# Performance work log

Measured on AMD Instinct MI355X. Metric: run time of the kernel, lower is better.

## Reference

```python
import jax, jax.numpy as jnp
import numpy as np

B, S, D_MODEL, H = 2, 2048, 1024, 16
HD = D_MODEL // H  # head_dim = 64


def setup_inputs() -> dict:
    key = jax.random.key(0)
    kx, kq, kk, kv, ko = jax.random.split(key, 5)
    scale = 1.0 / np.sqrt(D_MODEL)
    return {
        "x": jax.random.normal(kx, (B, S, D_MODEL), dtype=jnp.float32),
        "Wq": jax.random.normal(kq, (D_MODEL, D_MODEL), dtype=jnp.float32) * scale,
        "Wk": jax.random.normal(kk, (D_MODEL, D_MODEL), dtype=jnp.float32) * scale,
        "Wv": jax.random.normal(kv, (D_MODEL, D_MODEL), dtype=jnp.float32) * scale,
        "Wo": jax.random.normal(ko, (D_MODEL, D_MODEL), dtype=jnp.float32) * scale,
        "bo": jnp.zeros((D_MODEL,), dtype=jnp.float32),
    }


def reference(x, Wq, Wk, Wv, Wo, bo):
    b, s, _ = x.shape
    # project and split heads: [b, h, s, hd]
    q = (x @ Wq).reshape(b, s, H, HD).transpose(0, 2, 1, 3)
    k = (x @ Wk).reshape(b, s, H, HD).transpose(0, 2, 1, 3)
    v = (x @ Wv).reshape(b, s, H, HD).transpose(0, 2, 1, 3)
    # full attn score materialization, as in the original module
    scores = jnp.einsum("bhqd,bhkd->bhqk", q, k)
    causal = jnp.triu(jnp.ones((s, s), dtype=bool), k=1)  # True above diagonal -> masked
    scores = jnp.where(causal, -jnp.inf, scores)
    attn = jax.nn.softmax(scores / np.sqrt(HD), axis=-1)  # dropout p=0.0 (eval)
    ctx = jnp.einsum("bhqk,bhkd->bqhd", attn, v).reshape(b, s, D_MODEL)
    return ctx @ Wo + bo
```

## Files before the change

### kernel.cpp

```cpp
#include <hip/hip_runtime.h>
#include <stdint.h>

typedef __bf16 bf16x8 __attribute__((ext_vector_type(8)));
typedef float f32x4 __attribute__((ext_vector_type(4)));

static constexpr int B_ = 2, S_ = 2048, D_ = 1024, H_ = 16, HD_ = 64;
static constexpr int M_ = B_ * S_;
static constexpr size_t HSZ = (size_t)B_ * H_ * S_ * HD_;

#define DEV_INLINE __device__ __forceinline__

#define SC2F (0.125f * 1.4426950408889634f)

#define EXP2(x) __builtin_amdgcn_exp2f(x)

DEV_INLINE uint16_t f2bf(float f) {
  __bf16 h = (__bf16)f;
  return __builtin_bit_cast(uint16_t, h);
}
DEV_INLINE float bf2f(uint16_t u) {
  uint32_t x = (uint32_t)u << 16;
  return __builtin_bit_cast(float, x);
}
DEV_INLINE float fmax3(float a, float b, float c) { return fmaxf(fmaxf(a, b), c); }

#define GLD16(gptr, lptr)                                                        \
  __builtin_amdgcn_global_load_lds(                                              \
      (const __attribute__((address_space(1))) void*)(gptr),                     \
      (__attribute__((address_space(3))) void*)(lptr), 16, 0, 0)

__global__ void cvt_x_kernel(const float* __restrict__ x, uint16_t* __restrict__ xb) {
  int i = blockIdx.x * 256 + threadIdx.x;
  float4 v = reinterpret_cast<const float4*>(x)[i];
  ushort4 o;
  o.x = f2bf(v.x); o.y = f2bf(v.y); o.z = f2bf(v.z); o.w = f2bf(v.w);
  reinterpret_cast<ushort4*>(xb)[i] = o;
}

__global__ void tr_w_kernel(const float* __restrict__ W0, const float* __restrict__ W1,
                            const float* __restrict__ W2, const float* __restrict__ W3,
                            uint16_t* __restrict__ Wt) {
  __shared__ float tile[32][33];
  const float* W = (blockIdx.z == 0) ? W0 : (blockIdx.z == 1) ? W1
                   : (blockIdx.z == 2) ? W2 : W3;
  uint16_t* dst = Wt + (size_t)blockIdx.z * D_ * D_;
  int c = blockIdx.x * 32 + threadIdx.x;
  int r0 = blockIdx.y * 32;
#pragma unroll
  for (int j = threadIdx.y; j < 32; j += 8)
    tile[j][threadIdx.x] = W[(size_t)(r0 + j) * D_ + c];
  __syncthreads();
  int oc = blockIdx.y * 32 + threadIdx.x;
  int or0 = blockIdx.x * 32;
#pragma unroll
  for (int j = threadIdx.y; j < 32; j += 8)
    dst[(size_t)(or0 + j) * D_ + oc] = f2bf(tile[threadIdx.x][j]);
}

template <int EPI, int BM, int MINW>
__global__ __launch_bounds__(256, MINW)
void gemm_bt_kernel(const uint16_t* __restrict__ A, const uint16_t* __restrict__ Bt,
                    uint16_t* __restrict__ Cb, float* __restrict__ Cf,
                    const float* __restrict__ bias, int K, int gx, int chunk) {
  constexpr int MR = BM / 32;
  __shared__ uint16_t ldsA[2][BM * 32];
  __shared__ uint16_t ldsB[2][128 * 32];
  const int tid = threadIdx.x;
  const int lane = tid & 63;
  const int wid = tid >> 6;
  const int lo = lane & 15, hi = lane >> 4;

  const int id = blockIdx.x;
  const int tilei = (id & 7) * chunk + (id >> 3);
  const int bx = tilei % gx, by = tilei / gx;
  const int row0 = by * BM, col0 = bx * 128;
  const int wr = (wid >> 1) * (BM / 2), wc = (wid & 1) * 64;

  const uint16_t* gA = A + (size_t)(row0 + (tid >> 2)) * K + (tid & 3) * 8;
  const uint16_t* gB = Bt + (size_t)(col0 + (tid >> 2)) * K + (tid & 3) * 8;

  f32x4 acc[MR][4] = {};

  auto stage = [&](int kt, int buf) {
    const uint16_t* a = gA + kt * 32;
    const uint16_t* b = gB + kt * 32;
    char* la = (char*)&ldsA[buf][0] + tid * 16;
    char* lb = (char*)&ldsB[buf][0] + tid * 16;
    GLD16(a, la);
    if constexpr (BM == 128) GLD16(a + (size_t)64 * K, la + 4096);
    GLD16(b, lb);
    GLD16(b + (size_t)64 * K, lb + 4096);
  };

  const int nk = K >> 5;
  stage(0, 0);
  __syncthreads();
  for (int kt = 0; kt < nk; ++kt) {
    const int cur = kt & 1;
    if (kt + 1 < nk) stage(kt + 1, cur ^ 1);
    const uint16_t* lA = &ldsA[cur][0];
    const uint16_t* lB = &ldsB[cur][0];
    bf16x8 af[MR], bfr[4];
#pragma unroll
    for (int m = 0; m < MR; ++m)
      af[m] = *(const bf16x8*)(lA + (wr + m * 16 + lo) * 32 + hi * 8);
#pragma unroll
    for (int n = 0; n < 4; ++n)
      bfr[n] = *(const bf16x8*)(lB + (wc + n * 16 + lo) * 32 + hi * 8);
    __builtin_amdgcn_s_setprio(1);
#pragma unroll
    for (int m = 0; m < MR; ++m)
#pragma unroll
      for (int n = 0; n < 4; ++n)
        acc[m][n] = __builtin_amdgcn_mfma_f32_16x16x32_bf16(af[m], bfr[n], acc[m][n], 0, 0, 0);
    __builtin_amdgcn_s_setprio(0);
    __syncthreads();
  }

#pragma unroll
  for (int m = 0; m < MR; ++m)
#pragma unroll
    for (int n = 0; n < 4; ++n) {
      const int gr0 = row0 + wr + m * 16 + hi * 4;
      const int gc = col0 + wc + n * 16 + lo;
      if (EPI == 0) {
        const int which = gc >> 10, c = gc & 1023;
        const int hh = c >> 6, d = c & 63;
        const int bb = gr0 >> 11, s0 = gr0 & 2047;
        if (which == 2) {
          ushort4 pk;
          pk.x = f2bf(acc[m][n][0]); pk.y = f2bf(acc[m][n][1]);
          pk.z = f2bf(acc[m][n][2]); pk.w = f2bf(acc[m][n][3]);
          *reinterpret_cast<ushort4*>(
              &Cb[2 * HSZ + ((size_t)(bb * H_ + hh) * HD_ + d) * S_ + s0]) = pk;
        } else {
          const float qs = (which == 0) ? SC2F : 1.0f;
#pragma unroll
          for (int j = 0; j < 4; ++j)
            Cb[(size_t)which * HSZ + (((size_t)(bb * H_ + hh) * S_ + s0 + j) * HD_ + d)] =
                f2bf(acc[m][n][j] * qs);
        }
      } else {
#pragma unroll
        for (int j = 0; j < 4; ++j)
          Cf[(size_t)(gr0 + j) * D_ + gc] = acc[m][n][j] + bias[gc];
      }
    }
}

__global__ __launch_bounds__(256, 3)
void attn_kernel(const uint16_t* __restrict__ QKV, uint16_t* __restrict__ ctx,
                 uint16_t* __restrict__ Opart, float2* __restrict__ ml) {
  __shared__ uint16_t ldsKV[2][2][4096];
  __shared__ uint16_t ldsP[128][72];

  static const uint8_t jt[3][8] = {
      {0 << 2, 1 << 2, 2 << 2, 3 << 2, 4 << 2, 5 << 2, 6 << 2, (9 << 2) | 3},
      {(15 << 2) | 2, 7 << 2, (14 << 2) | 2, (14 << 2) | 3,
       (13 << 2) | 3, (12 << 2) | 3, (10 << 2) | 3, (11 << 2) | 2},
      {(15 << 2) | 3, (13 << 2) | 2, (12 << 2) | 2, (10 << 2) | 2,
       (9 << 2) | 2, (8 << 2) | 2, (8 << 2) | 3, (11 << 2) | 3},
  };

  const int tid = threadIdx.x;
  const int lane = tid & 63;
  const int w = tid >> 6;
  const int lo = lane & 15, hi = lane >> 4;
  const int swz = (hi * 8) ^ ((lo & 6) << 2);

  const int g = blockIdx.x;
  const int bh = g & 31, k = (g >> 5) & 7, r = g >> 8;
  const int j = jt[r][k];
  const int p = j >> 2;
  const bool split = (j & 2) != 0;
  const int c = j & 1;
  const int k0 = (split && c) ? (p + 1) : 0;
  const int k1 = (split && !c) ? (p + 1) : (2 * p + 2);
  const int h = bh & 15, b = bh >> 4;

  const size_t bhs = ((size_t)(b * H_ + h)) * S_ * HD_;
  const uint16_t* Q  = QKV + bhs;
  const uint16_t* Kp = QKV + HSZ + bhs;
  const uint16_t* Vt = QKV + 2 * HSZ + bhs;

  bf16x8 ones;
#pragma unroll
  for (int e = 0; e < 8; ++e) ones[e] = __builtin_bit_cast(__bf16, (uint16_t)0x3F80);

  const int srow = tid >> 2;
  const int scol = ((tid & 3) ^ ((tid >> 3) & 3)) * 8;
  auto stage = [&](int kt, int bufi) {
    const uint16_t* gk = Kp + (size_t)(kt * 64 + srow) * HD_ + scol;
    char* lk = (char*)&ldsKV[bufi][0][0] + tid * 16;
    GLD16(gk, lk);
    GLD16(gk + 32, lk + 4096);
    const uint16_t* gv = Vt + (size_t)srow * S_ + kt * 64 + scol;
    char* lv = (char*)&ldsKV[bufi][1][0] + tid * 16;
    GLD16(gv, lv);
    GLD16(gv + 32, lv + 4096);
  };

  const int q0w = p * 128 + w * 32;
  bf16x8 qf[2][2];
#pragma unroll
  for (int mm = 0; mm < 2; ++mm)
#pragma unroll
    for (int ks = 0; ks < 2; ++ks)
      qf[mm][ks] = *(const bf16x8*)(Q + (size_t)(q0w + mm * 16 + lo) * HD_ + ks * 32 + hi * 8);

  f32x4 acco[2][4] = {};
  f32x4 lacc[2] = {};
  float mstate[2] = {-1e30f, -1e30f};

  stage(k0, k0 & 1);
  asm volatile("s_waitcnt vmcnt(0)" ::: "memory");
  __builtin_amdgcn_s_barrier();
  __builtin_amdgcn_sched_barrier(0);

  for (int kt = k0; kt < k1; ++kt) {
    const int buf = kt & 1;
    if (kt + 1 < k1) stage(kt + 1, buf ^ 1);

    const bool active = (kt * 64) < (q0w + 32);
    if (active) {
      const uint16_t* lK = &ldsKV[buf][0][0];
      bf16x8 ak[4][2];
#pragma unroll
      for (int n = 0; n < 4; ++n)
#pragma unroll
        for (int ks = 0; ks < 2; ++ks)
          ak[n][ks] = *(const bf16x8*)(lK + ks * 2048 + (n * 16 + lo) * 32 + swz);

      f32x4 st[4][2];
      __builtin_amdgcn_s_setprio(1);
#pragma unroll
      for (int n = 0; n < 4; ++n)
#pragma unroll
        for (int mm = 0; mm < 2; ++mm) {
          f32x4 z = {};
          z = __builtin_amdgcn_mfma_f32_16x16x32_bf16(ak[n][0], qf[mm][0], z, 0, 0, 0);
          st[n][mm] = __builtin_amdgcn_mfma_f32_16x16x32_bf16(ak[n][1], qf[mm][1], z, 0, 0, 0);
        }
      __builtin_amdgcn_s_setprio(0);

      if (kt * 64 + 63 > q0w) {
#pragma unroll
        for (int n = 0; n < 4; ++n)
#pragma unroll
          for (int mm = 0; mm < 2; ++mm) {
            const int qg = q0w + mm * 16 + lo;
#pragma unroll
            for (int jj = 0; jj < 4; ++jj) {
              int kvg = kt * 64 + n * 16 + hi * 4 + jj;
              if (kvg > qg) st[n][mm][jj] = -1e30f;
            }
          }
      }

#pragma unroll
      for (int mm = 0; mm < 2; ++mm) {
        float t0 = fmax3(st[0][mm][0], st[0][mm][1], st[0][mm][2]);
        float t1 = fmax3(t0, st[0][mm][3], st[1][mm][0]);
        float t2 = fmax3(t1, st[1][mm][1], st[1][mm][2]);
        float t3 = fmax3(t2, st[1][mm][3], st[2][mm][0]);
        float t4 = fmax3(t3, st[2][mm][1], st[2][mm][2]);
        float t5 = fmax3(t4, st[2][mm][3], st[3][mm][0]);
        float t6 = fmax3(t5, st[3][mm][1], st[3][mm][2]);
        float vmax = fmaxf(t6, st[3][mm][3]);
        vmax = fmaxf(vmax, __shfl_xor(vmax, 16));
        vmax = fmaxf(vmax, __shfl_xor(vmax, 32));

        if (__any(vmax > mstate[mm] + 8.f)) {
          float mnew = fmaxf(mstate[mm], vmax);
          float sc = EXP2(mstate[mm] - mnew);
          mstate[mm] = mnew;
          lacc[mm] *= sc;
#pragma unroll
          for (int nd = 0; nd < 4; ++nd)
#pragma unroll
            for (int jj = 0; jj < 4; ++jj) acco[mm][nd][jj] *= sc;
        }

#pragma unroll
        for (int n = 0; n < 4; ++n) {
          ushort4 pk;
          pk.x = f2bf(EXP2(st[n][mm][0] - mstate[mm]));
          pk.y = f2bf(EXP2(st[n][mm][1] - mstate[mm]));
          pk.z = f2bf(EXP2(st[n][mm][2] - mstate[mm]));
          pk.w = f2bf(EXP2(st[n][mm][3] - mstate[mm]));
          *reinterpret_cast<ushort4*>(&ldsP[w * 32 + mm * 16 + lo][n * 16 + hi * 4]) = pk;
        }
      }

      const uint16_t* lV = &ldsKV[buf][1][0];
      bf16x8 ap[2][2], bv[4][2];
#pragma unroll
      for (int mm = 0; mm < 2; ++mm)
#pragma unroll
        for (int ks = 0; ks < 2; ++ks)
          ap[mm][ks] = *(const bf16x8*)(&ldsP[w * 32 + mm * 16 + lo][ks * 32 + hi * 8]);
#pragma unroll
      for (int nd = 0; nd < 4; ++nd)
#pragma unroll
        for (int ks = 0; ks < 2; ++ks)
          bv[nd][ks] = *(const bf16x8*)(lV + ks * 2048 + (nd * 16 + lo) * 32 + swz);
      __builtin_amdgcn_s_setprio(1);
#pragma unroll
      for (int mm = 0; mm < 2; ++mm) {
        lacc[mm] = __builtin_amdgcn_mfma_f32_16x16x32_bf16(ones, ap[mm][0], lacc[mm], 0, 0, 0);
        lacc[mm] = __builtin_amdgcn_mfma_f32_16x16x32_bf16(ones, ap[mm][1], lacc[mm], 0, 0, 0);
#pragma unroll
        for (int nd = 0; nd < 4; ++nd) {
          acco[mm][nd] = __builtin_amdgcn_mfma_f32_16x16x32_bf16(bv[nd][0], ap[mm][0], acco[mm][nd], 0, 0, 0);
          acco[mm][nd] = __builtin_amdgcn_mfma_f32_16x16x32_bf16(bv[nd][1], ap[mm][1], acco[mm][nd], 0, 0, 0);
        }
      }
      __builtin_amdgcn_s_setprio(0);
    }

    asm volatile("s_waitcnt vmcnt(0)" ::: "memory");
    __builtin_amdgcn_s_barrier();
    __builtin_amdgcn_sched_barrier(0);
  }

  if (!split) {
#pragma unroll
    for (int mm = 0; mm < 2; ++mm) {
      const float inv = 1.f / lacc[mm][0];
      uint16_t* crow = ctx + (size_t)(b * S_ + q0w + mm * 16 + lo) * D_ + h * HD_;
#pragma unroll
      for (int nd = 0; nd < 4; ++nd) {
        ushort4 pk;
        pk.x = f2bf(acco[mm][nd][0] * inv); pk.y = f2bf(acco[mm][nd][1] * inv);
        pk.z = f2bf(acco[mm][nd][2] * inv); pk.w = f2bf(acco[mm][nd][3] * inv);
        *reinterpret_cast<ushort4*>(crow + nd * 16 + hi * 4) = pk;
      }
    }
  } else {
    const int idx = ((bh * 8) + (p - 8)) * 2 + c;
    uint16_t* op = Opart + (size_t)idx * 8192;
#pragma unroll
    for (int mm = 0; mm < 2; ++mm) {
      const int qloc = w * 32 + mm * 16 + lo;
#pragma unroll
      for (int nd = 0; nd < 4; ++nd) {
        ushort4 pk;
        pk.x = f2bf(acco[mm][nd][0]); pk.y = f2bf(acco[mm][nd][1]);
        pk.z = f2bf(acco[mm][nd][2]); pk.w = f2bf(acco[mm][nd][3]);
        *reinterpret_cast<ushort4*>(op + qloc * 64 + nd * 16 + hi * 4) = pk;
      }
      if (hi == 0) ml[idx * 128 + qloc] = make_float2(mstate[mm], lacc[mm][0]);
    }
  }
}

__global__ void merge_kernel(const uint16_t* __restrict__ Opart,
                             const float2* __restrict__ ml,
                             uint16_t* __restrict__ ctx) {
  const int t = blockIdx.x * 256 + threadIdx.x;
  const int dh = t & 3, row = t >> 2;
  const int q = row & 127, si = (row >> 7) & 7, bh = row >> 10;
  const int h = bh & 15, b = bh >> 4;
  const int p = 8 + si;
  const int base = (bh * 8 + si) * 2;

  const float2 A = ml[base * 128 + q];
  const float2 Bv = ml[base * 128 + 128 + q];
  const float m = fmaxf(A.x, Bv.x);
  float sa = EXP2(A.x - m), sb = EXP2(Bv.x - m);
  const float inv = 1.f / (A.y * sa + Bv.y * sb);
  sa *= inv; sb *= inv;

  const uint16_t* Oa = Opart + (size_t)base * 8192 + q * 64 + dh * 16;
  const uint16_t* Ob = Oa + 8192;
  uint16_t* pc = ctx + ((size_t)(b * S_) + p * 128 + q) * D_ + h * HD_ + dh * 16;
#pragma unroll
  for (int hf = 0; hf < 2; ++hf) {
    int4 va = ((const int4*)Oa)[hf], vb = ((const int4*)Ob)[hf];
    const uint16_t* ua = (const uint16_t*)&va;
    const uint16_t* ub = (const uint16_t*)&vb;
    int4 vo;
    uint16_t* uo = (uint16_t*)&vo;
#pragma unroll
    for (int i = 0; i < 8; ++i)
      uo[i] = f2bf(bf2f(ua[i]) * sa + bf2f(ub[i]) * sb);
    ((int4*)pc)[hf] = vo;
  }
}

extern "C" void kernel_launch(void* const* d_in, const int* in_sizes, int n_in,
                              void* d_out, int out_size, void* d_ws, size_t ws_size,
                              hipStream_t stream) {
  (void)in_sizes; (void)n_in; (void)out_size; (void)ws_size;
  const float* x  = (const float*)d_in[0];
  const float* Wq = (const float*)d_in[1];
  const float* Wk = (const float*)d_in[2];
  const float* Wv = (const float*)d_in[3];
  const float* Wo = (const float*)d_in[4];
  const float* bo = (const float*)d_in[5];
  float* out = (float*)d_out;

  uint16_t* ws  = (uint16_t*)d_ws;
  uint16_t* xb  = ws;
  uint16_t* Wt  = xb + (size_t)M_ * D_;
  uint16_t* QKV = Wt + (size_t)4 * D_ * D_;
  uint16_t* ctx = QKV + 3 * HSZ;
  uint16_t* Opart = xb;
  float2*   mlbuf = (float2*)Wt;

  cvt_x_kernel<<<(M_ * D_) / 1024, 256, 0, stream>>>(x, xb);
  tr_w_kernel<<<dim3(32, 32, 4), dim3(32, 8), 0, stream>>>(Wq, Wk, Wv, Wo, Wt);
  gemm_bt_kernel<0, 128, 3><<<768, 256, 0, stream>>>(xb, Wt, QKV, nullptr, nullptr, D_, 24, 96);
  attn_kernel<<<768, 256, 0, stream>>>(QKV, ctx, Opart, mlbuf);
  merge_kernel<<<512, 256, 0, stream>>>(Opart, mlbuf, ctx);
  gemm_bt_kernel<1, 64, 2><<<512, 256, 0, stream>>>(ctx, Wt + (size_t)3 * D_ * D_, nullptr, out, bo, D_, 8, 64);
}
```

Measured before the change: 108.1 us.

## Load K tiles directly into registers with double-buffered prefetch instead of LDS

K fragments are now read from global memory straight into registers, using two register sets ping-ponged across a 2x unrolled loop, while only V is staged through LDS. This halves LDS traffic and footprint per iteration and removes the LDS reads for K. Each wave now loads the full K tile itself, so global/L2 traffic for K is multiplied by the four waves, and the extra register sets add VGPR pressure under the 3-block occupancy bound.

```diff
diff --git a/kernel.cpp b/kernel.cpp
--- a/kernel.cpp
+++ b/kernel.cpp
@@ -151,7 +151,7 @@
 __global__ __launch_bounds__(256, 3)
 void attn_kernel(const uint16_t* __restrict__ QKV, uint16_t* __restrict__ ctx,
                  uint16_t* __restrict__ Opart, float2* __restrict__ ml) {
-  __shared__ uint16_t ldsKV[2][2][4096];
+  __shared__ uint16_t ldsV[2][4096];
   __shared__ uint16_t ldsP[128][72];
 
   static const uint8_t jt[3][8] = {
@@ -190,16 +190,21 @@
   const int srow = tid >> 2;
   const int scol = ((tid & 3) ^ ((tid >> 3) & 3)) * 8;
   auto stage = [&](int kt, int bufi) {
-    const uint16_t* gk = Kp + (size_t)(kt * 64 + srow) * HD_ + scol;
-    char* lk = (char*)&ldsKV[bufi][0][0] + tid * 16;
-    GLD16(gk, lk);
-    GLD16(gk + 32, lk + 4096);
     const uint16_t* gv = Vt + (size_t)srow * S_ + kt * 64 + scol;
-    char* lv = (char*)&ldsKV[bufi][1][0] + tid * 16;
+    char* lv = (char*)&ldsV[bufi][0] + tid * 16;
     GLD16(gv, lv);
     GLD16(gv + 32, lv + 4096);
   };
 
+  auto loadK = [&](int kt, bf16x8 (&kr)[4][2]) {
+    const uint16_t* kb = Kp + (size_t)(kt * 64 + lo) * HD_ + hi * 8;
+#pragma unroll
+    for (int n = 0; n < 4; ++n)
+#pragma unroll
+      for (int ks = 0; ks < 2; ++ks)
+        kr[n][ks] = *(const bf16x8*)(kb + (size_t)n * 16 * HD_ + ks * 32);
+  };
+
   const int q0w = p * 128 + w * 32;
   bf16x8 qf[2][2];
 #pragma unroll
@@ -212,25 +217,22 @@
   f32x4 lacc[2] = {};
   float mstate[2] = {-1e30f, -1e30f};
 
+  bf16x8 kA[4][2], kB[4][2];
+  loadK(k0, kA);
   stage(k0, k0 & 1);
   asm volatile("s_waitcnt vmcnt(0)" ::: "memory");
   __builtin_amdgcn_s_barrier();
   __builtin_amdgcn_sched_barrier(0);
 
-  for (int kt = k0; kt < k1; ++kt) {
+  auto body = [&](bf16x8 (&kcur)[4][2], bf16x8 (&knxt)[4][2], int kt) {
     const int buf = kt & 1;
-    if (kt + 1 < k1) stage(kt + 1, buf ^ 1);
+    if (kt + 1 < k1) {
+      loadK(kt + 1, knxt);
+      stage(kt + 1, buf ^ 1);
+    }
 
     const bool active = (kt * 64) < (q0w + 32);
     if (active) {
-      const uint16_t* lK = &ldsKV[buf][0][0];
-      bf16x8 ak[4][2];
-#pragma unroll
-      for (int n = 0; n < 4; ++n)
-#pragma unroll
-        for (int ks = 0; ks < 2; ++ks)
-          ak[n][ks] = *(const bf16x8*)(lK + ks * 2048 + (n * 16 + lo) * 32 + swz);
-
       f32x4 st[4][2];
       __builtin_amdgcn_s_setprio(1);
 #pragma unroll
@@ -238,8 +240,8 @@
 #pragma unroll
         for (int mm = 0; mm < 2; ++mm) {
           f32x4 z = {};
-          z = __builtin_amdgcn_mfma_f32_16x16x32_bf16(ak[n][0], qf[mm][0], z, 0, 0, 0);
-          st[n][mm] = __builtin_amdgcn_mfma_f32_16x16x32_bf16(ak[n][1], qf[mm][1], z, 0, 0, 0);
+          z = __builtin_amdgcn_mfma_f32_16x16x32_bf16(kcur[n][0], qf[mm][0], z, 0, 0, 0);
+          st[n][mm] = __builtin_amdgcn_mfma_f32_16x16x32_bf16(kcur[n][1], qf[mm][1], z, 0, 0, 0);
         }
       __builtin_amdgcn_s_setprio(0);
 
@@ -292,7 +294,7 @@
         }
       }
 
-      const uint16_t* lV = &ldsKV[buf][1][0];
+      const uint16_t* lV = &ldsV[buf][0];
       bf16x8 ap[2][2], bv[4][2];
 #pragma unroll
       for (int mm = 0; mm < 2; ++mm)
@@ -321,6 +323,11 @@
     asm volatile("s_waitcnt vmcnt(0)" ::: "memory");
     __builtin_amdgcn_s_barrier();
     __builtin_amdgcn_sched_barrier(0);
+  };
+
+  for (int kt = k0; kt < k1; kt += 2) {
+    body(kA, kB, kt);
+    if (kt + 1 < k1) body(kB, kA, kt + 1);
   }
 
   if (!split) {
```

After: 144.6 us. +33.8%, slower.

## Use 256-row query tiles and split every tile's KV range in half

Applied to the files above, without the earlier changes.

The attention kernel now gives each block 256 query rows (64 per wave) instead of 128, so every staged K/V tile is reused across twice as many queries. Every query tile's KV range is split into two equal halves run by separate blocks, replacing the hand-tuned split table. The first half writes unnormalized output to ctx, the second to a partial buffer, and the merge kernel combines all tiles. This trades more register pressure (occupancy hint drops from 3 to 2) and a larger merge pass for fewer K/V loads per query.

```diff
diff --git a/kernel.cpp b/kernel.cpp
--- a/kernel.cpp
+++ b/kernel.cpp
@@ -148,18 +148,15 @@
     }
 }
 
-__global__ __launch_bounds__(256, 3)
+__global__ __launch_bounds__(256, 2)
 void attn_kernel(const uint16_t* __restrict__ QKV, uint16_t* __restrict__ ctx,
                  uint16_t* __restrict__ Opart, float2* __restrict__ ml) {
   __shared__ uint16_t ldsKV[2][2][4096];
-  __shared__ uint16_t ldsP[128][72];
-
-  static const uint8_t jt[3][8] = {
-      {0 << 2, 1 << 2, 2 << 2, 3 << 2, 4 << 2, 5 << 2, 6 << 2, (9 << 2) | 3},
-      {(15 << 2) | 2, 7 << 2, (14 << 2) | 2, (14 << 2) | 3,
-       (13 << 2) | 3, (12 << 2) | 3, (10 << 2) | 3, (11 << 2) | 2},
-      {(15 << 2) | 3, (13 << 2) | 2, (12 << 2) | 2, (10 << 2) | 2,
-       (9 << 2) | 2, (8 << 2) | 2, (8 << 2) | 3, (11 << 2) | 3},
+  __shared__ uint16_t ldsP[256][72];
+
+  static const uint8_t jt2[2][8] = {
+      {14, 15, 12, 13, 10, 11, 8, 9},
+      {0, 1, 2, 3, 4, 5, 6, 7},
   };
 
   const int tid = threadIdx.x;
@@ -170,12 +167,11 @@
 
   const int g = blockIdx.x;
   const int bh = g & 31, k = (g >> 5) & 7, r = g >> 8;
-  const int j = jt[r][k];
-  const int p = j >> 2;
-  const bool split = (j & 2) != 0;
-  const int c = j & 1;
-  const int k0 = (split && c) ? (p + 1) : 0;
-  const int k1 = (split && !c) ? (p + 1) : (2 * p + 2);
+  const int j = jt2[r][k];
+  const int p = j >> 1, c = j & 1;
+  const int half = 2 * (p + 1);
+  const int k0 = c ? half : 0;
+  const int k1 = c ? 2 * half : half;
   const int h = bh & 15, b = bh >> 4;
 
   const size_t bhs = ((size_t)(b * H_ + h)) * S_ * HD_;
@@ -200,17 +196,17 @@
     GLD16(gv + 32, lv + 4096);
   };
 
-  const int q0w = p * 128 + w * 32;
-  bf16x8 qf[2][2];
-#pragma unroll
-  for (int mm = 0; mm < 2; ++mm)
+  const int q0w = p * 256 + w * 64;
+  bf16x8 qf[4][2];
+#pragma unroll
+  for (int mm = 0; mm < 4; ++mm)
 #pragma unroll
     for (int ks = 0; ks < 2; ++ks)
       qf[mm][ks] = *(const bf16x8*)(Q + (size_t)(q0w + mm * 16 + lo) * HD_ + ks * 32 + hi * 8);
 
-  f32x4 acco[2][4] = {};
-  f32x4 lacc[2] = {};
-  float mstate[2] = {-1e30f, -1e30f};
+  f32x4 acco[4][4] = {};
+  f32x4 lacc[4] = {};
+  float mstate[4] = {-1e30f, -1e30f, -1e30f, -1e30f};
 
   stage(k0, k0 & 1);
   asm volatile("s_waitcnt vmcnt(0)" ::: "memory");
@@ -221,7 +217,7 @@
     const int buf = kt & 1;
     if (kt + 1 < k1) stage(kt + 1, buf ^ 1);
 
-    const bool active = (kt * 64) < (q0w + 32);
+    const bool active = (kt * 64) < (q0w + 64);
     if (active) {
       const uint16_t* lK = &ldsKV[buf][0][0];
       bf16x8 ak[4][2];
@@ -231,42 +227,39 @@
         for (int ks = 0; ks < 2; ++ks)
           ak[n][ks] = *(const bf16x8*)(lK + ks * 2048 + (n * 16 + lo) * 32 + swz);
 
-      f32x4 st[4][2];
-      __builtin_amdgcn_s_setprio(1);
-#pragma unroll
-      for (int n = 0; n < 4; ++n)
-#pragma unroll
-        for (int mm = 0; mm < 2; ++mm) {
+      const bool needMask = (kt * 64 + 63 > q0w);
+
+#pragma unroll
+      for (int mm = 0; mm < 4; ++mm) {
+        f32x4 st[4];
+        __builtin_amdgcn_s_setprio(1);
+#pragma unroll
+        for (int n = 0; n < 4; ++n) {
           f32x4 z = {};
           z = __builtin_amdgcn_mfma_f32_16x16x32_bf16(ak[n][0], qf[mm][0], z, 0, 0, 0);
-          st[n][mm] = __builtin_amdgcn_mfma_f32_16x16x32_bf16(ak[n][1], qf[mm][1], z, 0, 0, 0);
-        }
-      __builtin_amdgcn_s_setprio(0);
-
-      if (kt * 64 + 63 > q0w) {
-#pragma unroll
-        for (int n = 0; n < 4; ++n)
-#pragma unroll
-          for (int mm = 0; mm < 2; ++mm) {
-            const int qg = q0w + mm * 16 + lo;
+          st[n] = __builtin_amdgcn_mfma_f32_16x16x32_bf16(ak[n][1], qf[mm][1], z, 0, 0, 0);
+        }
+        __builtin_amdgcn_s_setprio(0);
+
+        if (needMask) {
+          const int qg = q0w + mm * 16 + lo;
+#pragma unroll
+          for (int n = 0; n < 4; ++n)
 #pragma unroll
             for (int jj = 0; jj < 4; ++jj) {
               int kvg = kt * 64 + n * 16 + hi * 4 + jj;
-              if (kvg > qg) st[n][mm][jj] = -1e30f;
+              if (kvg > qg) st[n][jj] = -1e30f;
             }
-          }
-      }
-
-#pragma unroll
-      for (int mm = 0; mm < 2; ++mm) {
-        float t0 = fmax3(st[0][mm][0], st[0][mm][1], st[0][mm][2]);
-        float t1 = fmax3(t0, st[0][mm][3], st[1][mm][0]);
-        float t2 = fmax3(t1, st[1][mm][1], st[1][mm][2]);
-        float t3 = fmax3(t2, st[1][mm][3], st[2][mm][0]);
-        float t4 = fmax3(t3, st[2][mm][1], st[2][mm][2]);
-        float t5 = fmax3(t4, st[2][mm][3], st[3][mm][0]);
-        float t6 = fmax3(t5, st[3][mm][1], st[3][mm][2]);
-        float vmax = fmaxf(t6, st[3][mm][3]);
+        }
+
+        float t0 = fmax3(st[0][0], st[0][1], st[0][2]);
+        float t1 = fmax3(t0, st[0][3], st[1][0]);
+        float t2 = fmax3(t1, st[1][1], st[1][2]);
+        float t3 = fmax3(t2, st[1][3], st[2][0]);
+        float t4 = fmax3(t3, st[2][1], st[2][2]);
+        float t5 = fmax3(t4, st[2][3], st[3][0]);
+        float t6 = fmax3(t5, st[3][1], st[3][2]);
+        float vmax = fmaxf(t6, st[3][3]);
         vmax = fmaxf(vmax, __shfl_xor(vmax, 16));
         vmax = fmaxf(vmax, __shfl_xor(vmax, 32));
 
@@ -284,38 +277,35 @@
 #pragma unroll
         for (int n = 0; n < 4; ++n) {
           ushort4 pk;
-          pk.x = f2bf(EXP2(st[n][mm][0] - mstate[mm]));
-          pk.y = f2bf(EXP2(st[n][mm][1] - mstate[mm]));
-          pk.z = f2bf(EXP2(st[n][mm][2] - mstate[mm]));
-          pk.w = f2bf(EXP2(st[n][mm][3] - mstate[mm]));
-          *reinterpret_cast<ushort4*>(&ldsP[w * 32 + mm * 16 + lo][n * 16 + hi * 4]) = pk;
+          pk.x = f2bf(EXP2(st[n][0] - mstate[mm]));
+          pk.y = f2bf(EXP2(st[n][1] - mstate[mm]));
+          pk.z = f2bf(EXP2(st[n][2] - mstate[mm]));
+          pk.w = f2bf(EXP2(st[n][3] - mstate[mm]));
+          *reinterpret_cast<ushort4*>(&ldsP[w * 64 + mm * 16 + lo][n * 16 + hi * 4]) = pk;
         }
       }
 
       const uint16_t* lV = &ldsKV[buf][1][0];
-      bf16x8 ap[2][2], bv[4][2];
-#pragma unroll
-      for (int mm = 0; mm < 2; ++mm)
-#pragma unroll
-        for (int ks = 0; ks < 2; ++ks)
-          ap[mm][ks] = *(const bf16x8*)(&ldsP[w * 32 + mm * 16 + lo][ks * 32 + hi * 8]);
+      bf16x8 bv[4][2];
 #pragma unroll
       for (int nd = 0; nd < 4; ++nd)
 #pragma unroll
         for (int ks = 0; ks < 2; ++ks)
           bv[nd][ks] = *(const bf16x8*)(lV + ks * 2048 + (nd * 16 + lo) * 32 + swz);
-      __builtin_amdgcn_s_setprio(1);
-#pragma unroll
-      for (int mm = 0; mm < 2; ++mm) {
-        lacc[mm] = __builtin_amdgcn_mfma_f32_16x16x32_bf16(ones, ap[mm][0], lacc[mm], 0, 0, 0);
-        lacc[mm] = __builtin_amdgcn_mfma_f32_16x16x32_bf16(ones, ap[mm][1], lacc[mm], 0, 0, 0);
+#pragma unroll
+      for (int mm = 0; mm < 4; ++mm) {
+        bf16x8 ap0 = *(const bf16x8*)(&ldsP[w * 64 + mm * 16 + lo][hi * 8]);
+        bf16x8 ap1 = *(const bf16x8*)(&ldsP[w * 64 + mm * 16 + lo][32 + hi * 8]);
+        __builtin_amdgcn_s_setprio(1);
+        lacc[mm] = __builtin_amdgcn_mfma_f32_16x16x32_bf16(ones, ap0, lacc[mm], 0, 0, 0);
+        lacc[mm] = __builtin_amdgcn_mfma_f32_16x16x32_bf16(ones, ap1, lacc[mm], 0, 0, 0);
 #pragma unroll
         for (int nd = 0; nd < 4; ++nd) {
-          acco[mm][nd] = __builtin_amdgcn_mfma_f32_16x16x32_bf16(bv[nd][0], ap[mm][0], acco[mm][nd], 0, 0, 0);
-          acco[mm][nd] = __builtin_amdgcn_mfma_f32_16x16x32_bf16(bv[nd][1], ap[mm][1], acco[mm][nd], 0, 0, 0);
-        }
+          acco[mm][nd] = __builtin_amdgcn_mfma_f32_16x16x32_bf16(bv[nd][0], ap0, acco[mm][nd], 0, 0, 0);
+          acco[mm][nd] = __builtin_amdgcn_mfma_f32_16x16x32_bf16(bv[nd][1], ap1, acco[mm][nd], 0, 0, 0);
+        }
+        __builtin_amdgcn_s_setprio(0);
       }
-      __builtin_amdgcn_s_setprio(0);
     }
 
     asm volatile("s_waitcnt vmcnt(0)" ::: "memory");
@@ -323,34 +313,23 @@
     __builtin_amdgcn_sched_barrier(0);
   }
 
-  if (!split) {
-#pragma unroll
-    for (int mm = 0; mm < 2; ++mm) {
-      const float inv = 1.f / lacc[mm][0];
-      uint16_t* crow = ctx + (size_t)(b * S_ + q0w + mm * 16 + lo) * D_ + h * HD_;
-#pragma unroll
-      for (int nd = 0; nd < 4; ++nd) {
-        ushort4 pk;
-        pk.x = f2bf(acco[mm][nd][0] * inv); pk.y = f2bf(acco[mm][nd][1] * inv);
-        pk.z = f2bf(acco[mm][nd][2] * inv); pk.w = f2bf(acco[mm][nd][3] * inv);
-        *reinterpret_cast<ushort4*>(crow + nd * 16 + hi * 4) = pk;
-      }
+  const int idx = bh * 8 + p;
+#pragma unroll
+  for (int mm = 0; mm < 4; ++mm) {
+    const int qloc = w * 64 + mm * 16 + lo;
+    uint16_t* dst;
+    if (c == 0)
+      dst = ctx + (size_t)(b * S_ + p * 256 + qloc) * D_ + h * HD_;
+    else
+      dst = Opart + (size_t)idx * 16384 + (size_t)qloc * 64;
+#pragma unroll
+    for (int nd = 0; nd < 4; ++nd) {
+      ushort4 pk;
+      pk.x = f2bf(acco[mm][nd][0]); pk.y = f2bf(acco[mm][nd][1]);
+      pk.z = f2bf(acco[mm][nd][2]); pk.w = f2bf(acco[mm][nd][3]);
+      *reinterpret_cast<ushort4*>(dst + nd * 16 + hi * 4) = pk;
     }
-  } else {
-    const int idx = ((bh * 8) + (p - 8)) * 2 + c;
-    uint16_t* op = Opart + (size_t)idx * 8192;
-#pragma unroll
-    for (int mm = 0; mm < 2; ++mm) {
-      const int qloc = w * 32 + mm * 16 + lo;
-#pragma unroll
-      for (int nd = 0; nd < 4; ++nd) {
-        ushort4 pk;
-        pk.x = f2bf(acco[mm][nd][0]); pk.y = f2bf(acco[mm][nd][1]);
-        pk.z = f2bf(acco[mm][nd][2]); pk.w = f2bf(acco[mm][nd][3]);
-        *reinterpret_cast<ushort4*>(op + qloc * 64 + nd * 16 + hi * 4) = pk;
-      }
-      if (hi == 0) ml[idx * 128 + qloc] = make_float2(mstate[mm], lacc[mm][0]);
-    }
+    if (hi == 0) ml[(idx * 2 + c) * 256 + qloc] = make_float2(mstate[mm], lacc[mm][0]);
   }
 }
 
@@ -359,24 +338,22 @@
                              uint16_t* __restrict__ ctx) {
   const int t = blockIdx.x * 256 + threadIdx.x;
   const int dh = t & 3, row = t >> 2;
-  const int q = row & 127, si = (row >> 7) & 7, bh = row >> 10;
+  const int q = row & 255, p = (row >> 8) & 7, bh = row >> 11;
   const int h = bh & 15, b = bh >> 4;
-  const int p = 8 + si;
-  const int base = (bh * 8 + si) * 2;
-
-  const float2 A = ml[base * 128 + q];
-  const float2 Bv = ml[base * 128 + 128 + q];
+  const int idx = bh * 8 + p;
+
+  const float2 A = ml[(idx * 2 + 0) * 256 + q];
+  const float2 Bv = ml[(idx * 2 + 1) * 256 + q];
   const float m = fmaxf(A.x, Bv.x);
   float sa = EXP2(A.x - m), sb = EXP2(Bv.x - m);
   const float inv = 1.f / (A.y * sa + Bv.y * sb);
   sa *= inv; sb *= inv;
 
-  const uint16_t* Oa = Opart + (size_t)base * 8192 + q * 64 + dh * 16;
-  const uint16_t* Ob = Oa + 8192;
-  uint16_t* pc = ctx + ((size_t)(b * S_) + p * 128 + q) * D_ + h * HD_ + dh * 16;
+  uint16_t* pc = ctx + ((size_t)(b * S_) + p * 256 + q) * D_ + h * HD_ + dh * 16;
+  const uint16_t* pb = Opart + (size_t)idx * 16384 + (size_t)q * 64 + dh * 16;
 #pragma unroll
   for (int hf = 0; hf < 2; ++hf) {
-    int4 va = ((const int4*)Oa)[hf], vb = ((const int4*)Ob)[hf];
+    int4 va = ((const int4*)pc)[hf], vb = ((const int4*)pb)[hf];
     const uint16_t* ua = (const uint16_t*)&va;
     const uint16_t* ub = (const uint16_t*)&vb;
     int4 vo;
@@ -411,7 +388,7 @@
   cvt_x_kernel<<<(M_ * D_) / 1024, 256, 0, stream>>>(x, xb);
   tr_w_kernel<<<dim3(32, 32, 4), dim3(32, 8), 0, stream>>>(Wq, Wk, Wv, Wo, Wt);
   gemm_bt_kernel<0, 128, 3><<<768, 256, 0, stream>>>(xb, Wt, QKV, nullptr, nullptr, D_, 24, 96);
-  attn_kernel<<<768, 256, 0, stream>>>(QKV, ctx, Opart, mlbuf);
-  merge_kernel<<<512, 256, 0, stream>>>(Opart, mlbuf, ctx);
+  attn_kernel<<<512, 256, 0, stream>>>(QKV, ctx, Opart, mlbuf);
+  merge_kernel<<<1024, 256, 0, stream>>>(Opart, mlbuf, ctx);
   gemm_bt_kernel<1, 64, 2><<<512, 256, 0, stream>>>(ctx, Wt + (size_t)3 * D_ * D_, nullptr, out, bo, D_, 8, 64);
 }
```

Result: slower. 119.2 us (+10.3%).
